# Performance work log

Hardware: AMD Instinct MI355X
Metric: run time of the kernel (lower is better)

The kernel has to match this reference:

```python
import jax, jax.numpy as jnp
import numpy as np

N_GENES = 5000
BATCH = 32
N_EDGES = 80000
H1, H2, LATENT = 64, 64, 64


def setup_inputs() -> dict:
    key = jax.random.key(0)
    ks = jax.random.split(key, 8)
    x = jax.random.normal(ks[0], (BATCH, N_GENES), dtype=jnp.float32)
    edge_index = jax.random.randint(ks[1], (2, N_EDGES), 0, N_GENES, dtype=jnp.int64)
    # GCNConv weights (PyG lin: y = x @ W^T, stored here as [in, out]) + bias
    def xavier(k, shape):
        fan_in, fan_out = shape
        lim = jnp.sqrt(6.0 / (fan_in + fan_out)).astype(jnp.float32)
        return jax.random.uniform(k, shape, jnp.float32, -lim, lim)
    W1 = xavier(ks[2], (1, H1));   b1 = jnp.zeros((H1,), jnp.float32)
    W2 = xavier(ks[3], (H1, H2));  b2 = jnp.zeros((H2,), jnp.float32)
    Wmu = xavier(ks[4], (H2, LATENT));  bmu = jnp.zeros((LATENT,), jnp.float32)
    Wlv = xavier(ks[5], (H2, LATENT));  blv = jnp.zeros((LATENT,), jnp.float32)
    return {"x": x, "edge_index": edge_index, "W1": W1, "b1": b1,
            "W2": W2, "b2": b2, "Wmu": Wmu, "bmu": bmu, "Wlv": Wlv, "blv": blv}


def _gcn_norm(edge_index, num_nodes):
    # Add self loops, compute symmetric normalization D^-1/2 (A+I) D^-1/2
    loop = jnp.arange(num_nodes, dtype=edge_index.dtype)
    src = jnp.concatenate([edge_index[0], loop])
    dst = jnp.concatenate([edge_index[1], loop])
    deg = jax.ops.segment_sum(jnp.ones_like(src, dtype=jnp.float32), dst,
                              num_segments=num_nodes)
    dinv = jnp.where(deg > 0, 1.0 / jnp.sqrt(deg), 0.0)
    norm = dinv[src] * dinv[dst]  # [E + N]
    return src, dst, norm


def _gcn_conv(h, src, dst, norm, W, b, num_nodes):
    # h: [N, B, Fin] (node-major so segment_sum vectorizes over batch)
    h = h @ W                                    # [N, B, Fout]
    msg = h[src] * norm[:, None, None]           # gather + scale: [E+N, B, Fout]
    agg = jax.ops.segment_sum(msg, dst, num_segments=num_nodes)  # scatter-add
    return agg + b


def reference(x, edge_index, W1, b1, W2, b2, Wmu, bmu, Wlv, blv):
    B, N = x.shape
    src, dst, norm = _gcn_norm(edge_index, N)
    h = x.T[:, :, None]                          # [N, B, 1]
    h = jax.nn.relu(_gcn_conv(h, src, dst, norm, W1, b1, N))
    h = jax.nn.relu(_gcn_conv(h, src, dst, norm, W2, b2, N))
    gene_embeddings = jnp.transpose(h, (1, 0, 2))  # [B, N, H2]
    pooled = jnp.mean(gene_embeddings, axis=1)     # [B, H2]
    mu = pooled @ Wmu + bmu
    logvar = pooled @ Wlv + blv
    return mu, logvar, gene_embeddings
```

## Files before the change

### kernel.cpp

```cpp
#include <hip/hip_runtime.h>
#include <hip/hip_bf16.h>

#define N_NODES 5000
#define N_EDGES 80000
#define BATCH   32
#define FDIM    64
#define BF      (BATCH * FDIM)

#define OFF_DEG      0
#define OFF_FILL     20480
#define OFF_POOLED   40960
#define ZERO_BYTES   49152
#define OFF_DINV     49408
#define OFF_ROWPTR   69632
#define OFF_EDGES    90112
#define OFF_COL      730112
#define OFF_VAL      1050112
#define OFF_XT       1370112
#define OFF_S        2010112

__global__ void k_edges(const unsigned int* __restrict__ raw,
                        int* __restrict__ edges, int* __restrict__ deg) {
    unsigned int hi = raw[2 * (threadIdx.x & 63) + 1];
    bool is64 = (__ballot(hi == 0u) == ~0ull);
    int i = blockIdx.x * 256 + threadIdx.x;
    if (i < 2 * N_EDGES) {
        int v = is64 ? (int)raw[2 * i] : (int)raw[i];
        edges[i] = v;
        if (i >= N_EDGES) atomicAdd(&deg[v], 1);
    }
}

__global__ void k_scan(const int* __restrict__ deg, int* __restrict__ row_ptr,
                       float* __restrict__ dinv) {
    __shared__ int part[1024];
    int tid = threadIdx.x;
    int base = tid * 5;
    int local[5];
    int sum = 0;
    for (int i = 0; i < 5; i++) {
        int idx = base + i;
        int v = 0;
        if (idx < N_NODES) {
            v = deg[idx];
            dinv[idx] = 1.0f / sqrtf((float)v + 1.0f);
        }
        local[i] = sum;
        sum += v;
    }
    part[tid] = sum;
    __syncthreads();
    for (int off = 1; off < 1024; off <<= 1) {
        int v = (tid >= off) ? part[tid - off] : 0;
        __syncthreads();
        part[tid] += v;
        __syncthreads();
    }
    int prefix = (tid > 0) ? part[tid - 1] : 0;
    for (int i = 0; i < 5; i++) {
        int idx = base + i;
        if (idx < N_NODES) row_ptr[idx] = prefix + local[i];
    }
    if (tid == 1023) row_ptr[N_NODES] = part[1023];
}

__global__ void k_fill(const int* __restrict__ edges, const int* __restrict__ row_ptr,
                       int* __restrict__ fill, const float* __restrict__ dinv,
                       int* __restrict__ col, float* __restrict__ val) {
    int e = blockIdx.x * 256 + threadIdx.x;
    if (e >= N_EDGES) return;
    int s = edges[e];
    int d = edges[N_EDGES + e];
    int pos = atomicAdd(&fill[d], 1);
    int idx = row_ptr[d] + pos;
    col[idx] = s;
    val[idx] = dinv[s] * dinv[d];
}

__global__ void k_transpose(const float* __restrict__ x, float* __restrict__ xT) {
    int i = blockIdx.x * 256 + threadIdx.x;
    if (i >= BATCH * N_NODES) return;
    int b = i / N_NODES, n = i % N_NODES;
    xT[n * BATCH + b] = x[i];
}

__global__ __launch_bounds__(256) void k_spmm1(const float* __restrict__ xT,
                                               const int* __restrict__ row_ptr,
                                               const int* __restrict__ col,
                                               const float* __restrict__ val,
                                               const float* __restrict__ dinv,
                                               float* __restrict__ s_out) {
    int g = threadIdx.x >> 5;
    int lane = threadIdx.x & 31;
    int n = blockIdx.x * 8 + g;
    if (n >= N_NODES) return;
    float dv = dinv[n];
    float acc = dv * dv * xT[n * BATCH + lane];
    int beg = row_ptr[n], end = row_ptr[n + 1];
    for (int i = beg; i < end; i += 8) {
        float pv[8], wv[8];
#pragma unroll
        for (int u = 0; u < 8; u++) {
            int e = i + u;
            int c = (e < end) ? col[e] : n;
            wv[u] = (e < end) ? val[e] : 0.0f;
            pv[u] = xT[c * BATCH + lane];
        }
#pragma unroll
        for (int u = 0; u < 8; u++) acc = fmaf(wv[u], pv[u], acc);
    }
    s_out[n * BATCH + lane] = acc;
}

__global__ __launch_bounds__(256) void k_l2fused(const float* __restrict__ s,
                                                 const int* __restrict__ row_ptr,
                                                 const int* __restrict__ col,
                                                 const float* __restrict__ val,
                                                 const float* __restrict__ dinv,
                                                 const float* __restrict__ W1,
                                                 const float* __restrict__ b1,
                                                 const float* __restrict__ W2,
                                                 const float* __restrict__ b2,
                                                 float* __restrict__ out) {
    __shared__ float w2s[64 * 64];
    __shared__ float aggs[FDIM][BATCH];
    int n = blockIdx.x;
    int g = threadIdx.x >> 5, b = threadIdx.x & 31;

    const float4* W2v4 = (const float4*)W2;
    float4* w2s4 = (float4*)w2s;
#pragma unroll
    for (int u = 0; u < 4; u++)
        w2s4[u * 256 + threadIdx.x] = W2v4[u * 256 + threadIdx.x];

    float w1r[8], b1r[8];
#pragma unroll
    for (int j = 0; j < 8; j++) { w1r[j] = W1[g * 8 + j]; b1r[j] = b1[g * 8 + j]; }

    float dv = dinv[n];
    float dv2 = dv * dv;
    float sv0 = s[n * BATCH + b];
    float acc[8];
#pragma unroll
    for (int j = 0; j < 8; j++)
        acc[j] = dv2 * fmaxf(fmaf(sv0, w1r[j], b1r[j]), 0.0f);

    int beg = row_ptr[n], end = row_ptr[n + 1];
    for (int i = beg; i < end; i += 8) {
        float sv[8], wv[8];
#pragma unroll
        for (int u = 0; u < 8; u++) {
            int e = i + u;
            int c = (e < end) ? col[e] : n;
            wv[u] = (e < end) ? val[e] : 0.0f;
            sv[u] = s[c * BATCH + b];
        }
#pragma unroll
        for (int u = 0; u < 8; u++)
#pragma unroll
            for (int j = 0; j < 8; j++)
                acc[j] = fmaf(wv[u], fmaxf(fmaf(sv[u], w1r[j], b1r[j]), 0.0f), acc[j]);
    }
#pragma unroll
    for (int j = 0; j < 8; j++) aggs[g * 8 + j][b] = acc[j];
    __syncthreads();

    float o[8];
#pragma unroll
    for (int j = 0; j < 8; j++) o[j] = b2[g * 8 + j];
#pragma unroll 8
    for (int k = 0; k < 64; k++) {
        float hv = aggs[k][b];
        float4 wa = *(const float4*)&w2s[k * 64 + g * 8];
        float4 wb = *(const float4*)&w2s[k * 64 + g * 8 + 4];
        o[0] = fmaf(hv, wa.x, o[0]); o[1] = fmaf(hv, wa.y, o[1]);
        o[2] = fmaf(hv, wa.z, o[2]); o[3] = fmaf(hv, wa.w, o[3]);
        o[4] = fmaf(hv, wb.x, o[4]); o[5] = fmaf(hv, wb.y, o[5]);
        o[6] = fmaf(hv, wb.z, o[6]); o[7] = fmaf(hv, wb.w, o[7]);
    }
    float4 r0, r1;
    r0.x = fmaxf(o[0], 0.f); r0.y = fmaxf(o[1], 0.f);
    r0.z = fmaxf(o[2], 0.f); r0.w = fmaxf(o[3], 0.f);
    r1.x = fmaxf(o[4], 0.f); r1.y = fmaxf(o[5], 0.f);
    r1.z = fmaxf(o[6], 0.f); r1.w = fmaxf(o[7], 0.f);
    float* op = out + 2 * BF + (size_t)b * (N_NODES * FDIM) + n * FDIM + g * 8;
    ((float4*)op)[0] = r0;
    ((float4*)op)[1] = r1;
}

__global__ __launch_bounds__(256) void k_pooled(const float* __restrict__ out,
                                                float* __restrict__ pooled) {
    int bid = blockIdx.x;
    int b = bid / 40, chunk = bid % 40;
    int sub = threadIdx.x >> 6;
    int f = threadIdx.x & 63;
    const float* g = out + 2 * BF + (size_t)b * (N_NODES * FDIM) + (chunk * 125) * FDIM + f;
    int r0 = sub * 32;
    int r1 = r0 + 32; if (r1 > 125) r1 = 125;
    float acc = 0.f;
    for (int r = r0; r < r1; r++) acc += g[r * FDIM];
    atomicAdd(&pooled[b * FDIM + f], acc);
}

__global__ void k_head(const float* __restrict__ pooled, const float* __restrict__ Wmu,
                       const float* __restrict__ bmu, const float* __restrict__ Wlv,
                       const float* __restrict__ blv, float* __restrict__ out) {
    int id = blockIdx.x * 256 + threadIdx.x;
    if (id >= BF) return;
    int b = id >> 6, f = id & 63;
    const float sc = 1.0f / 5000.0f;
    float mu = bmu[f], lv = blv[f];
    for (int k = 0; k < 64; k++) {
        float p = pooled[b * 64 + k] * sc;
        mu = fmaf(p, Wmu[k * 64 + f], mu);
        lv = fmaf(p, Wlv[k * 64 + f], lv);
    }
    out[id] = mu;
    out[BF + id] = lv;
}

extern "C" void kernel_launch(void* const* d_in, const int* in_sizes, int n_in,
                              void* d_out, int out_size, void* d_ws, size_t ws_size,
                              hipStream_t stream) {
    const float* x   = (const float*)d_in[0];
    const int*   era = (const int*)d_in[1];
    const float* W1  = (const float*)d_in[2];
    const float* b1  = (const float*)d_in[3];
    const float* W2  = (const float*)d_in[4];
    const float* b2  = (const float*)d_in[5];
    const float* Wmu = (const float*)d_in[6];
    const float* bmu = (const float*)d_in[7];
    const float* Wlv = (const float*)d_in[8];
    const float* blv = (const float*)d_in[9];
    float* out = (float*)d_out;
    char*  ws  = (char*)d_ws;

    int*   deg    = (int*)(ws + OFF_DEG);
    int*   fill   = (int*)(ws + OFF_FILL);
    float* pooled = (float*)(ws + OFF_POOLED);
    float* dinv   = (float*)(ws + OFF_DINV);
    int*   rowp   = (int*)(ws + OFF_ROWPTR);
    int*   edges  = (int*)(ws + OFF_EDGES);
    int*   col    = (int*)(ws + OFF_COL);
    float* val    = (float*)(ws + OFF_VAL);
    float* xT     = (float*)(ws + OFF_XT);
    float* s      = (float*)(ws + OFF_S);

    hipMemsetAsync(ws, 0, ZERO_BYTES, stream);
    k_edges<<<625, 256, 0, stream>>>((const unsigned int*)era, edges, deg);
    k_transpose<<<625, 256, 0, stream>>>(x, xT);
    k_scan<<<1, 1024, 0, stream>>>(deg, rowp, dinv);
    k_fill<<<313, 256, 0, stream>>>(edges, rowp, fill, dinv, col, val);
    k_spmm1<<<625, 256, 0, stream>>>(xT, rowp, col, val, dinv, s);
    k_l2fused<<<5000, 256, 0, stream>>>(s, rowp, col, val, dinv, W1, b1, W2, b2, out);
    k_pooled<<<1280, 256, 0, stream>>>(out, pooled);
    k_head<<<8, 256, 0, stream>>>(pooled, Wmu, bmu, Wlv, blv, out);
}
```

Measured before the change: 174.1 us.

## Use split-bf16 MFMA for W2 matmul and fuse pooling into layer-2 kernel

Replaces the scalar FMA W2 matmul in the fused layer-2 kernel with bf16 MFMA instructions. Both operands are split into hi/lo bf16 parts (three MFMAs per tile) to keep close to fp32 accuracy, and W2 is pre-split and transposed in a merged preprocessing kernel that also absorbs the transpose kernel. The separate pooling pass, which re-read the whole embedding output, is replaced by atomic adds into 64 spread partial buffers that the head kernel then reduces. The cost is a larger memset and many global atomics, plus a small accuracy change from the bf16 splitting.

```diff
diff --git a/kernel.cpp b/kernel.cpp
--- a/kernel.cpp
+++ b/kernel.cpp
@@ -6,21 +6,39 @@
 #define BATCH   32
 #define FDIM    64
 #define BF      (BATCH * FDIM)
+#define NSPREAD 64
 
 #define OFF_DEG      0
 #define OFF_FILL     20480
-#define OFF_POOLED   40960
-#define ZERO_BYTES   49152
-#define OFF_DINV     49408
-#define OFF_ROWPTR   69632
-#define OFF_EDGES    90112
-#define OFF_COL      730112
-#define OFF_VAL      1050112
-#define OFF_XT       1370112
-#define OFF_S        2010112
-
-__global__ void k_edges(const unsigned int* __restrict__ raw,
-                        int* __restrict__ edges, int* __restrict__ deg) {
+#define OFF_POOLEDP  40960
+#define ZERO_BYTES   565248
+#define OFF_DINV     565248
+#define OFF_ROWPTR   585728
+#define OFF_EDGES    606208
+#define OFF_COL      1246208
+#define OFF_VAL      1566208
+#define OFF_XT       1886208
+#define OFF_S        2526208
+#define OFF_W2H      3166208
+#define OFF_W2L      3174400
+
+typedef __attribute__((ext_vector_type(8))) short short8;
+typedef __attribute__((ext_vector_type(4))) float f32x4;
+
+__device__ inline short f2bf(float f) {
+    unsigned u = __builtin_bit_cast(unsigned, f);
+    unsigned r = (u + 0x7fffu + ((u >> 16) & 1u)) >> 16;
+    return (short)r;
+}
+__device__ inline float bf2f(short h) {
+    unsigned u = ((unsigned)(unsigned short)h) << 16;
+    return __builtin_bit_cast(float, u);
+}
+
+__global__ void k_pre(const unsigned int* __restrict__ raw, const float* __restrict__ x,
+                      const float* __restrict__ W2, int* __restrict__ edges,
+                      int* __restrict__ deg, float* __restrict__ xT,
+                      short* __restrict__ w2hT, short* __restrict__ w2lT) {
     unsigned int hi = raw[2 * (threadIdx.x & 63) + 1];
     bool is64 = (__ballot(hi == 0u) == ~0ull);
     int i = blockIdx.x * 256 + threadIdx.x;
@@ -28,6 +46,17 @@
         int v = is64 ? (int)raw[2 * i] : (int)raw[i];
         edges[i] = v;
         if (i >= N_EDGES) atomicAdd(&deg[v], 1);
+    }
+    if (i < BATCH * N_NODES) {
+        int b = i / N_NODES, n = i % N_NODES;
+        xT[n * BATCH + b] = x[i];
+    }
+    if (i < FDIM * FDIM) {
+        float w = W2[i];
+        int k = i >> 6, f = i & 63;
+        short h = f2bf(w);
+        w2hT[f * 64 + k] = h;
+        w2lT[f * 64 + k] = f2bf(w - bf2f(h));
     }
 }
 
@@ -75,13 +104,6 @@
     int idx = row_ptr[d] + pos;
     col[idx] = s;
     val[idx] = dinv[s] * dinv[d];
-}
-
-__global__ void k_transpose(const float* __restrict__ x, float* __restrict__ xT) {
-    int i = blockIdx.x * 256 + threadIdx.x;
-    if (i >= BATCH * N_NODES) return;
-    int b = i / N_NODES, n = i % N_NODES;
-    xT[n * BATCH + b] = x[i];
 }
 
 __global__ __launch_bounds__(256) void k_spmm1(const float* __restrict__ xT,
@@ -119,19 +141,14 @@
                                                  const float* __restrict__ dinv,
                                                  const float* __restrict__ W1,
                                                  const float* __restrict__ b1,
-                                                 const float* __restrict__ W2,
+                                                 const short* __restrict__ w2hT,
+                                                 const short* __restrict__ w2lT,
                                                  const float* __restrict__ b2,
-                                                 float* __restrict__ out) {
-    __shared__ float w2s[64 * 64];
+                                                 float* __restrict__ out,
+                                                 float* __restrict__ pooledP) {
     __shared__ float aggs[FDIM][BATCH];
     int n = blockIdx.x;
     int g = threadIdx.x >> 5, b = threadIdx.x & 31;
-
-    const float4* W2v4 = (const float4*)W2;
-    float4* w2s4 = (float4*)w2s;
-#pragma unroll
-    for (int u = 0; u < 4; u++)
-        w2s4[u * 256 + threadIdx.x] = W2v4[u * 256 + threadIdx.x];
 
     float w1r[8], b1r[8];
 #pragma unroll
@@ -151,9 +168,9 @@
 #pragma unroll
         for (int u = 0; u < 8; u++) {
             int e = i + u;
-            int c = (e < end) ? col[e] : n;
+            int c2 = (e < end) ? col[e] : n;
             wv[u] = (e < end) ? val[e] : 0.0f;
-            sv[u] = s[c * BATCH + b];
+            sv[u] = s[c2 * BATCH + b];
         }
 #pragma unroll
         for (int u = 0; u < 8; u++)
@@ -165,58 +182,75 @@
     for (int j = 0; j < 8; j++) aggs[g * 8 + j][b] = acc[j];
     __syncthreads();
 
-    float o[8];
-#pragma unroll
-    for (int j = 0; j < 8; j++) o[j] = b2[g * 8 + j];
+    int lane = threadIdx.x & 63;
+    int wave = threadIdx.x >> 6;
+    int c = lane & 15, q = lane >> 4;
+    int mt = wave >> 1;
+    int nt0 = (wave & 1) * 2;
+
+    short8 bh[2][2], bl[2][2];
+#pragma unroll
+    for (int nti = 0; nti < 2; nti++)
+#pragma unroll
+        for (int kt = 0; kt < 2; kt++) {
+            int f = (nt0 + nti) * 16 + c;
+            bh[nti][kt] = *(const short8*)&w2hT[f * 64 + kt * 32 + q * 8];
+            bl[nti][kt] = *(const short8*)&w2lT[f * 64 + kt * 32 + q * 8];
+        }
+    short8 ah[2], al[2];
+    int brow = mt * 16 + c;
+#pragma unroll
+    for (int kt = 0; kt < 2; kt++)
+#pragma unroll
+        for (int j = 0; j < 8; j++) {
+            float a = aggs[kt * 32 + q * 8 + j][brow];
+            short h = f2bf(a);
+            ah[kt][j] = h;
+            al[kt][j] = f2bf(a - bf2f(h));
+        }
+    f32x4 dacc[2];
+#pragma unroll
+    for (int nti = 0; nti < 2; nti++) dacc[nti] = (f32x4){0.f, 0.f, 0.f, 0.f};
+#pragma unroll
+    for (int nti = 0; nti < 2; nti++)
+#pragma unroll
+        for (int kt = 0; kt < 2; kt++) {
+            dacc[nti] = __builtin_amdgcn_mfma_f32_16x16x32_bf16(al[kt], bh[nti][kt], dacc[nti], 0, 0, 0);
+            dacc[nti] = __builtin_amdgcn_mfma_f32_16x16x32_bf16(ah[kt], bl[nti][kt], dacc[nti], 0, 0, 0);
+            dacc[nti] = __builtin_amdgcn_mfma_f32_16x16x32_bf16(ah[kt], bh[nti][kt], dacc[nti], 0, 0, 0);
+        }
+#pragma unroll
+    for (int nti = 0; nti < 2; nti++) {
+        int f = (nt0 + nti) * 16 + c;
+        float bias = b2[f];
+#pragma unroll
+        for (int r = 0; r < 4; r++) {
+            int bb = mt * 16 + q * 4 + r;
+            float v = fmaxf(dacc[nti][r] + bias, 0.0f);
+            out[2 * BF + (size_t)bb * (N_NODES * FDIM) + n * FDIM + f] = v;
+            atomicAdd(&pooledP[(n & (NSPREAD - 1)) * BF + bb * 64 + f], v);
+        }
+    }
+}
+
+__global__ void k_head(const float* __restrict__ pooledP, const float* __restrict__ Wmu,
+                       const float* __restrict__ bmu, const float* __restrict__ Wlv,
+                       const float* __restrict__ blv, float* __restrict__ out) {
+    __shared__ float pb[64];
+    int b = blockIdx.x, f = threadIdx.x;
+    float acc = 0.f;
+    for (int c = 0; c < NSPREAD; c++) acc += pooledP[c * BF + b * 64 + f];
+    pb[f] = acc * (1.0f / 5000.0f);
+    __syncthreads();
+    float mu = bmu[f], lv = blv[f];
 #pragma unroll 8
     for (int k = 0; k < 64; k++) {
-        float hv = aggs[k][b];
-        float4 wa = *(const float4*)&w2s[k * 64 + g * 8];
-        float4 wb = *(const float4*)&w2s[k * 64 + g * 8 + 4];
-        o[0] = fmaf(hv, wa.x, o[0]); o[1] = fmaf(hv, wa.y, o[1]);
-        o[2] = fmaf(hv, wa.z, o[2]); o[3] = fmaf(hv, wa.w, o[3]);
-        o[4] = fmaf(hv, wb.x, o[4]); o[5] = fmaf(hv, wb.y, o[5]);
-        o[6] = fmaf(hv, wb.z, o[6]); o[7] = fmaf(hv, wb.w, o[7]);
-    }
-    float4 r0, r1;
-    r0.x = fmaxf(o[0], 0.f); r0.y = fmaxf(o[1], 0.f);
-    r0.z = fmaxf(o[2], 0.f); r0.w = fmaxf(o[3], 0.f);
-    r1.x = fmaxf(o[4], 0.f); r1.y = fmaxf(o[5], 0.f);
-    r1.z = fmaxf(o[6], 0.f); r1.w = fmaxf(o[7], 0.f);
-    float* op = out + 2 * BF + (size_t)b * (N_NODES * FDIM) + n * FDIM + g * 8;
-    ((float4*)op)[0] = r0;
-    ((float4*)op)[1] = r1;
-}
-
-__global__ __launch_bounds__(256) void k_pooled(const float* __restrict__ out,
-                                                float* __restrict__ pooled) {
-    int bid = blockIdx.x;
-    int b = bid / 40, chunk = bid % 40;
-    int sub = threadIdx.x >> 6;
-    int f = threadIdx.x & 63;
-    const float* g = out + 2 * BF + (size_t)b * (N_NODES * FDIM) + (chunk * 125) * FDIM + f;
-    int r0 = sub * 32;
-    int r1 = r0 + 32; if (r1 > 125) r1 = 125;
-    float acc = 0.f;
-    for (int r = r0; r < r1; r++) acc += g[r * FDIM];
-    atomicAdd(&pooled[b * FDIM + f], acc);
-}
-
-__global__ void k_head(const float* __restrict__ pooled, const float* __restrict__ Wmu,
-                       const float* __restrict__ bmu, const float* __restrict__ Wlv,
-                       const float* __restrict__ blv, float* __restrict__ out) {
-    int id = blockIdx.x * 256 + threadIdx.x;
-    if (id >= BF) return;
-    int b = id >> 6, f = id & 63;
-    const float sc = 1.0f / 5000.0f;
-    float mu = bmu[f], lv = blv[f];
-    for (int k = 0; k < 64; k++) {
-        float p = pooled[b * 64 + k] * sc;
+        float p = pb[k];
         mu = fmaf(p, Wmu[k * 64 + f], mu);
         lv = fmaf(p, Wlv[k * 64 + f], lv);
     }
-    out[id] = mu;
-    out[BF + id] = lv;
+    out[b * 64 + f] = mu;
+    out[BF + b * 64 + f] = lv;
 }
 
 extern "C" void kernel_launch(void* const* d_in, const int* in_sizes, int n_in,
@@ -235,24 +269,24 @@
     float* out = (float*)d_out;
     char*  ws  = (char*)d_ws;
 
-    int*   deg    = (int*)(ws + OFF_DEG);
-    int*   fill   = (int*)(ws + OFF_FILL);
-    float* pooled = (float*)(ws + OFF_POOLED);
-    float* dinv   = (float*)(ws + OFF_DINV);
-    int*   rowp   = (int*)(ws + OFF_ROWPTR);
-    int*   edges  = (int*)(ws + OFF_EDGES);
-    int*   col    = (int*)(ws + OFF_COL);
-    float* val    = (float*)(ws + OFF_VAL);
-    float* xT     = (float*)(ws + OFF_XT);
-    float* s      = (float*)(ws + OFF_S);
+    int*   deg     = (int*)(ws + OFF_DEG);
+    int*   fill    = (int*)(ws + OFF_FILL);
+    float* pooledP = (float*)(ws + OFF_POOLEDP);
+    float* dinv    = (float*)(ws + OFF_DINV);
+    int*   rowp    = (int*)(ws + OFF_ROWPTR);
+    int*   edges   = (int*)(ws + OFF_EDGES);
+    int*   col     = (int*)(ws + OFF_COL);
+    float* val     = (float*)(ws + OFF_VAL);
+    float* xT      = (float*)(ws + OFF_XT);
+    float* s       = (float*)(ws + OFF_S);
+    short* w2hT    = (short*)(ws + OFF_W2H);
+    short* w2lT    = (short*)(ws + OFF_W2L);
 
     hipMemsetAsync(ws, 0, ZERO_BYTES, stream);
-    k_edges<<<625, 256, 0, stream>>>((const unsigned int*)era, edges, deg);
-    k_transpose<<<625, 256, 0, stream>>>(x, xT);
+    k_pre<<<625, 256, 0, stream>>>((const unsigned int*)era, x, W2, edges, deg, xT, w2hT, w2lT);
     k_scan<<<1, 1024, 0, stream>>>(deg, rowp, dinv);
     k_fill<<<313, 256, 0, stream>>>(edges, rowp, fill, dinv, col, val);
     k_spmm1<<<625, 256, 0, stream>>>(xT, rowp, col, val, dinv, s);
-    k_l2fused<<<5000, 256, 0, stream>>>(s, rowp, col, val, dinv, W1, b1, W2, b2, out);
-    k_pooled<<<1280, 256, 0, stream>>>(out, pooled);
-    k_head<<<8, 256, 0, stream>>>(pooled, Wmu, bmu, Wlv, blv, out);
-}
+    k_l2fused<<<5000, 256, 0, stream>>>(s, rowp, col, val, dinv, W1, b1, w2hT, w2lT, b2, out, pooledP);
+    k_head<<<32, 64, 0, stream>>>(pooledP, Wmu, bmu, Wlv, blv, out);
+}
```

Measured after the change: 158.8 us. -8.8%, faster.
